# Kernel optimization log

Hardware: AMD Instinct MI355X
Metric: run time of the kernel (lower is better)

Reference implementation:

```python
import jax, jax.numpy as jnp
import numpy as np

D_MODEL = 1024
NUM_HEADS = 16
MAX_SEQ_LEN = 2048
BATCH = 4
SEQ_LEN = 2048


def setup_inputs() -> dict:
    key = jax.random.key(0)
    ks = jax.random.split(key, 7)
    s = 0.02
    return {
        "x": jax.random.normal(ks[0], (BATCH, SEQ_LEN, D_MODEL), dtype=jnp.float32),
        "Wq": jax.random.normal(ks[1], (D_MODEL, D_MODEL), dtype=jnp.float32) * s,
        "Wk": jax.random.normal(ks[2], (D_MODEL, D_MODEL), dtype=jnp.float32) * s,
        "Wv": jax.random.normal(ks[3], (D_MODEL, D_MODEL), dtype=jnp.float32) * s,
        "Wo": jax.random.normal(ks[4], (D_MODEL, D_MODEL), dtype=jnp.float32) * s,
        "bo": jnp.zeros((D_MODEL,), dtype=jnp.float32),
        "bias_table": jax.random.normal(ks[5], (2 * MAX_SEQ_LEN - 1, NUM_HEADS), dtype=jnp.float32) * s,
    }


def reference(x, Wq, Wk, Wv, Wo, bo, bias_table):
    B, S, D = x.shape
    H = NUM_HEADS
    hd = D // H
    scale = hd ** -0.5

    # torch Linear: y = x @ W.T
    q = (x @ Wq.T).reshape(B, S, H, hd).transpose(0, 2, 1, 3)  # [B,H,S,hd]
    k = (x @ Wk.T).reshape(B, S, H, hd).transpose(0, 2, 1, 3)
    v = (x @ Wv.T).reshape(B, S, H, hd).transpose(0, 2, 1, 3)

    scores = jnp.einsum("bhqd,bhkd->bhqk", q, k) * scale  # [B,H,S,S]

    # relative index: coords[:,None] - coords[None,:] + max_seq_len - 1
    coords = jnp.arange(S)
    rel_idx = coords[:, None] - coords[None, :] + MAX_SEQ_LEN - 1  # [S,S]
    rel_bias = bias_table[rel_idx]              # [S,S,H]
    rel_bias = rel_bias.transpose(2, 0, 1)[None]  # [1,H,S,S]

    probs = jax.nn.softmax(scores + rel_bias, axis=-1)
    ctx = jnp.einsum("bhqk,bhkd->bhqd", probs, v)  # [B,H,S,hd]
    ctx = ctx.transpose(0, 2, 1, 3).reshape(B, S, D)
    return ctx @ Wo.T + bo
```

## Files before the change

### kernel.cpp

```cpp
#include <hip/hip_runtime.h>
#include <string.h>

typedef unsigned short u16;
typedef unsigned int   u32;
typedef __attribute__((ext_vector_type(8))) short short8;
typedef __attribute__((ext_vector_type(4))) float f32x4;
typedef __attribute__((ext_vector_type(16))) float f32x16;
typedef __attribute__((ext_vector_type(2))) __fp16 h2;
typedef __attribute__((ext_vector_type(8))) __fp16 h8;
typedef __attribute__((ext_vector_type(2))) unsigned int u32x2;

__device__ __forceinline__ u16 f2b(float f) {
  u32 u = __float_as_uint(f);
  u32 r = (u + 0x7fffu + ((u >> 16) & 1u)) >> 16;
  return (u16)r;
}
__device__ __forceinline__ void cp16(const u16* g, u16* l) {
  __builtin_amdgcn_global_load_lds(
      (const __attribute__((address_space(1))) void*)g,
      (__attribute__((address_space(3))) void*)l, 16, 0, 0);
}
__device__ __forceinline__ void plswap(u32& a, u32& b) {
  u32x2 r = __builtin_amdgcn_permlane32_swap(a, b, false, false);
  a = r[0]; b = r[1];
}

__global__ __launch_bounds__(256) void cvt_f2b_kernel(const float* __restrict__ in,
                                                      u16* __restrict__ out, int n) {
  int i = (blockIdx.x * 256 + threadIdx.x) * 4;
  if (i + 3 < n) {
    float4 v = *(const float4*)&in[i];
    ushort4 o = make_ushort4(f2b(v.x), f2b(v.y), f2b(v.z), f2b(v.w));
    *(ushort4*)&out[i] = o;
  }
}
__global__ __launch_bounds__(256) void cvtw_kernel(const float* __restrict__ w0,
                                                   const float* __restrict__ w1,
                                                   const float* __restrict__ w2,
                                                   const float* __restrict__ w3,
                                                   u16* __restrict__ out) {
  const float* src = (blockIdx.y == 0) ? w0 : (blockIdx.y == 1) ? w1
                   : (blockIdx.y == 2) ? w2 : w3;
  int i = (blockIdx.x * 256 + threadIdx.x) * 4;
  float4 v = *(const float4*)&src[i];
  ushort4 o = make_ushort4(f2b(v.x), f2b(v.y), f2b(v.z), f2b(v.w));
  *(ushort4*)&out[(size_t)blockIdx.y * 1048576 + i] = o;
}

template<int MODE>
__global__ __launch_bounds__(256) void gemm128_bt(
    const u16* __restrict__ A, const u16* __restrict__ Bw,
    void* __restrict__ outp, const float* __restrict__ bias,
    const int M, const int N, const int K) {
  __shared__ __attribute__((aligned(16))) u16 As[2][128 * 32];
  __shared__ __attribute__((aligned(16))) u16 Bs[2][128 * 32];

  const u16* Bw2 = Bw;
  if (MODE == 0) Bw2 += ((size_t)blockIdx.z) << 20;

  const int tid  = threadIdx.x;
  const int wave = tid >> 6, lane = tid & 63;
  const int quad = lane >> 4, l15 = lane & 15;
  const int wm   = (wave >> 1) * 64, wn = (wave & 1) * 64;
  const int m0   = blockIdx.x * 128, n0 = blockIdx.y * 128;

  const int srow = wave * 32 + (lane >> 2);
  const int scol = (lane & 3) * 8;
  const u16* gA0 = A   + (size_t)(m0 + srow) * K + scol;
  const u16* gA1 = gA0 + (size_t)16 * K;
  const u16* gB0 = Bw2 + (size_t)(n0 + srow) * K + scol;
  const u16* gB1 = gB0 + (size_t)16 * K;
  const int lo0 = (wave * 32) * 32, lo1 = (wave * 32 + 16) * 32;

  cp16(gA0, &As[0][lo0]); cp16(gA1, &As[0][lo1]);
  cp16(gB0, &Bs[0][lo0]); cp16(gB1, &Bs[0][lo1]);
  gA0 += 32; gA1 += 32; gB0 += 32; gB1 += 32;

  f32x4 acc[4][4] = {};
  const int nk = K >> 5;
  for (int kt = 0; kt < nk; ++kt) {
    const int cur = kt & 1;
    __syncthreads();
    if (kt + 1 < nk) {
      cp16(gA0, &As[1 - cur][lo0]); cp16(gA1, &As[1 - cur][lo1]);
      cp16(gB0, &Bs[1 - cur][lo0]); cp16(gB1, &Bs[1 - cur][lo1]);
      gA0 += 32; gA1 += 32; gB0 += 32; gB1 += 32;
    }
    short8 af[4], bf[4];
    #pragma unroll
    for (int mi = 0; mi < 4; ++mi)
      af[mi] = *(const short8*)&As[cur][(wm + mi * 16 + l15) * 32 + quad * 8];
    #pragma unroll
    for (int ni = 0; ni < 4; ++ni)
      bf[ni] = *(const short8*)&Bs[cur][(wn + ni * 16 + l15) * 32 + quad * 8];
    #pragma unroll
    for (int mi = 0; mi < 4; ++mi)
      #pragma unroll
      for (int ni = 0; ni < 4; ++ni)
        acc[mi][ni] = __builtin_amdgcn_mfma_f32_16x16x32_bf16(af[mi], bf[ni], acc[mi][ni], 0, 0, 0);
  }

  #pragma unroll
  for (int mi = 0; mi < 4; ++mi)
    #pragma unroll
    for (int ni = 0; ni < 4; ++ni) {
      if (MODE == 0 && blockIdx.z == 2) {
        int mb = m0 + wm + mi * 16 + quad * 4;
        int n  = n0 + wn + ni * 16 + l15;
        int b = mb >> 11, s = mb & 2047, h = n >> 6, d = n & 63;
        u16* out = (u16*)outp + (((size_t)2) << 23);
        h2 p0 = __builtin_amdgcn_cvt_pkrtz(acc[mi][ni][0], acc[mi][ni][1]);
        h2 p1 = __builtin_amdgcn_cvt_pkrtz(acc[mi][ni][2], acc[mi][ni][3]);
        ushort4 o;
        memcpy(&o.x, &p0, 4);
        memcpy(&o.z, &p1, 4);
        *(ushort4*)&out[((((size_t)b * 16 + h) * 64 + d) << 11) + s] = o;
      } else {
        #pragma unroll
        for (int r = 0; r < 4; ++r) {
          int m = m0 + wm + mi * 16 + quad * 4 + r;
          int n = n0 + wn + ni * 16 + l15;
          float v = acc[mi][ni][r];
          if (MODE == 0) {
            int b = m >> 11, s = m & 2047, h = n >> 6, d = n & 63;
            u16* out = (u16*)outp + (((size_t)blockIdx.z) << 23);
            out[((((size_t)b * 16 + h) * 2048 + s) << 6) + d] = f2b(v);
          } else {
            ((float*)outp)[(size_t)m * N + n] = v + bias[n];
          }
        }
      }
    }
}

__global__ __launch_bounds__(256, 2) void attn_mfma_kernel(
    const u16* __restrict__ qb, const u16* __restrict__ kb, const u16* __restrict__ vtb,
    const float* __restrict__ bias_table, u16* __restrict__ ctx) {
  __shared__ __attribute__((aligned(16))) u16 Ks[2][64 * 64];
  __shared__ __attribute__((aligned(16))) u16 Vs[2][64 * 64];
  __shared__ __attribute__((aligned(16))) f32x4 bias4[2304];

  const int tid  = threadIdx.x;
  const int wave = tid >> 6, lane = tid & 63;
  const int l31  = lane & 31, hi = lane >> 5;
  const int xsw  = l31 & 7;
  const int bh   = blockIdx.x, h = bh & 15, b = bh >> 4;
  const int q0   = blockIdx.y * 256;

  {
    float* btmp = (float*)&Ks[0][0];
    for (int i = tid; i < 2304; i += 256) {
      int j = q0 + i; if (j > 4094) j = 4094;
      btmp[i] = bias_table[j * 16 + h] * 1.44269504f;
    }
    __syncthreads();
    for (int i = tid; i < 2304; i += 256) {
      f32x4 v;
      v[0] = btmp[i];
      v[1] = btmp[(i + 1) & 2047 ? (i + 1 < 2304 ? i + 1 : 2303) : (i + 1 < 2304 ? i + 1 : 2303)];
      v[1] = btmp[i + 1 < 2304 ? i + 1 : 2303];
      v[2] = btmp[i + 2 < 2304 ? i + 2 : 2303];
      v[3] = btmp[i + 3 < 2304 ? i + 3 : 2303];
      bias4[i] = v;
    }
    __syncthreads();
  }

  short8 aQ[2][4];
  #pragma unroll
  for (int qs = 0; qs < 2; ++qs)
    #pragma unroll
    for (int ks = 0; ks < 4; ++ks)
      aQ[qs][ks] = *(const short8*)&qb[((size_t)bh * 2048 + q0 + wave * 64 + qs * 32 + l31) * 64
                                       + ks * 16 + hi * 8];

  f32x16 accO[2][2] = {};
  f32x16 accL[2]    = {};

  const h8 ones8 = {(__fp16)1.f, (__fp16)1.f, (__fp16)1.f, (__fp16)1.f,
                    (__fp16)1.f, (__fp16)1.f, (__fp16)1.f, (__fp16)1.f};

  const int krow = lane >> 3;
  const int kchk = (lane & 7) ^ krow;
  const u16* kbase = kb + (((size_t)bh * 2048) << 6);

  const int srow = tid >> 2, t0 = tid & 3, ssw = srow & 7;
  const u16* vrow = vtb + (((size_t)bh * 64 + srow) << 11) + t0 * 16;
  const int vo0 = srow * 64 + (((2 * t0    ) ^ ssw) << 3);
  const int vo1 = srow * 64 + (((2 * t0 + 1) ^ ssw) << 3);

  short8 vpre0 = *(const short8*)&vrow[0];
  short8 vpre1 = *(const short8*)&vrow[8];
  *(short8*)&Vs[0][vo0] = vpre0;
  *(short8*)&Vs[0][vo1] = vpre1;
  #pragma unroll
  for (int g = 0; g < 2; ++g)
    cp16(kbase + (size_t)(wave * 16 + g * 8 + krow) * 64 + kchk * 8,
         &Ks[0][(wave * 16 + g * 8) * 64]);
  vpre0 = *(const short8*)&vrow[64];
  vpre1 = *(const short8*)&vrow[72];

  for (int kt = 0; kt < 32; ++kt) {
    const int cur = kt & 1;
    __syncthreads();
    if (kt < 31) {
      #pragma unroll
      for (int g = 0; g < 2; ++g)
        cp16(kbase + (size_t)((kt + 1) * 64 + wave * 16 + g * 8 + krow) * 64 + kchk * 8,
             &Ks[1 - cur][(wave * 16 + g * 8) * 64]);
      *(short8*)&Vs[1 - cur][vo0] = vpre0;
      *(short8*)&Vs[1 - cur][vo1] = vpre1;
      if (kt < 30) {
        const u16* vp = vrow + ((size_t)(kt + 2) << 6);
        vpre0 = *(const short8*)&vp[0];
        vpre1 = *(const short8*)&vp[8];
      }
    }

    #pragma unroll
    for (int t = 0; t < 2; ++t) {
      short8 aK[4];
      #pragma unroll
      for (int ks = 0; ks < 4; ++ks)
        aK[ks] = *(const short8*)&Ks[cur][(t * 32 + l31) * 64
                                          + (((ks * 2 + hi) ^ xsw) << 3)];
      f32x16 accS[2] = {};
      __builtin_amdgcn_s_setprio(1);
      #pragma unroll
      for (int ks = 0; ks < 4; ++ks)
        #pragma unroll
        for (int qs = 0; qs < 2; ++qs)
          accS[qs] = __builtin_amdgcn_mfma_f32_32x32x16_bf16(aK[ks], aQ[qs][ks], accS[qs], 0, 0, 0);
      __builtin_amdgcn_s_setprio(0);

      u32 d[2][8];
      #pragma unroll
      for (int qs = 0; qs < 2; ++qs) {
        const int ib3 = wave * 64 + qs * 32 + l31 - kt * 64 - t * 32 - 4 * hi + 2044;
        #pragma unroll
        for (int rg = 0; rg < 4; ++rg) {
          const f32x4 bb4 = bias4[ib3 - 8 * rg];
          float p0 = __builtin_amdgcn_exp2f(fmaf(accS[qs][4 * rg + 0], 0.18033688f, bb4[3]));
          float p1 = __builtin_amdgcn_exp2f(fmaf(accS[qs][4 * rg + 1], 0.18033688f, bb4[2]));
          float p2 = __builtin_amdgcn_exp2f(fmaf(accS[qs][4 * rg + 2], 0.18033688f, bb4[1]));
          float p3 = __builtin_amdgcn_exp2f(fmaf(accS[qs][4 * rg + 3], 0.18033688f, bb4[0]));
          h2 e0; e0[0] = (__fp16)p0; e0[1] = (__fp16)p1;
          h2 e1; e1[0] = (__fp16)p2; e1[1] = (__fp16)p3;
          memcpy(&d[qs][2 * rg],     &e0, 4);
          memcpy(&d[qs][2 * rg + 1], &e1, 4);
        }
      }

      #pragma unroll
      for (int sl = 0; sl < 2; ++sl) {
        const int ch = ((t * 2 + sl) * 2 + hi) ^ xsw;
        short8 av0 = *(const short8*)&Vs[cur][(     l31) * 64 + (ch << 3)];
        short8 av1 = *(const short8*)&Vs[cur][(32 + l31) * 64 + (ch << 3)];
        h8 avh0, avh1;
        memcpy(&avh0, &av0, 16);
        memcpy(&avh1, &av1, 16);
        __builtin_amdgcn_s_setprio(1);
        #pragma unroll
        for (int qs = 0; qs < 2; ++qs) {
          u32 F0 = d[qs][4 * sl], F1 = d[qs][4 * sl + 1];
          u32 F2 = d[qs][4 * sl + 2], F3 = d[qs][4 * sl + 3];
          plswap(F0, F2);
          plswap(F1, F3);
          union { u32 w[4]; h8 v; } uf;
          uf.w[0] = F0; uf.w[1] = F1; uf.w[2] = F2; uf.w[3] = F3;
          accO[qs][0] = __builtin_amdgcn_mfma_f32_32x32x16_f16(avh0, uf.v, accO[qs][0], 0, 0, 0);
          accO[qs][1] = __builtin_amdgcn_mfma_f32_32x32x16_f16(avh1, uf.v, accO[qs][1], 0, 0, 0);
          accL[qs]    = __builtin_amdgcn_mfma_f32_32x32x16_f16(ones8, uf.v, accL[qs], 0, 0, 0);
        }
        __builtin_amdgcn_s_setprio(0);
      }
    }
  }

  #pragma unroll
  for (int qs = 0; qs < 2; ++qs) {
    const float inv = 1.0f / accL[qs][0];
    const int q = q0 + wave * 64 + qs * 32 + l31;
    #pragma unroll
    for (int dt = 0; dt < 2; ++dt)
      #pragma unroll
      for (int rg = 0; rg < 4; ++rg) {
        ushort4 o = make_ushort4(f2b(accO[qs][dt][4 * rg + 0] * inv), f2b(accO[qs][dt][4 * rg + 1] * inv),
                                 f2b(accO[qs][dt][4 * rg + 2] * inv), f2b(accO[qs][dt][4 * rg + 3] * inv));
        *(ushort4*)&ctx[((size_t)b * 2048 + q) * 1024 + h * 64 + dt * 32 + rg * 8 + hi * 4] = o;
      }
  }
}

extern "C" void kernel_launch(void* const* d_in, const int* in_sizes, int n_in,
                              void* d_out, int out_size, void* d_ws, size_t ws_size,
                              hipStream_t stream) {
  const float* x          = (const float*)d_in[0];
  const float* Wq         = (const float*)d_in[1];
  const float* Wk         = (const float*)d_in[2];
  const float* Wv         = (const float*)d_in[3];
  const float* Wo         = (const float*)d_in[4];
  const float* bo         = (const float*)d_in[5];
  const float* bias_table = (const float*)d_in[6];
  float* out = (float*)d_out;

  char* ws = (char*)d_ws;
  u16* xb   = (u16*)(ws);
  u16* wqb  = (u16*)(ws + 16777216);
  u16* wob  = (u16*)(ws + 16777216 + 3 * 2097152);
  u16* qb   = (u16*)(ws + 25165824);
  u16* kb   = qb + 8388608;
  u16* vtb  = kb + 8388608;
  u16* ctxb = (u16*)(ws + 75497472);

  cvt_f2b_kernel<<<8192, 256, 0, stream>>>(x, xb, 8388608);
  cvtw_kernel<<<dim3(1024, 4), 256, 0, stream>>>(Wq, Wk, Wv, Wo, wqb);

  gemm128_bt<0><<<dim3(64, 8, 3), 256, 0, stream>>>(
      xb, wqb, (void*)qb, nullptr, 8192, 1024, 1024);

  attn_mfma_kernel<<<dim3(64, 8), 256, 0, stream>>>(qb, kb, vtb, bias_table, ctxb);

  gemm128_bt<1><<<dim3(64, 8), 256, 0, stream>>>(
      ctxb, wob, (void*)out, bo, 8192, 1024, 1024);
}
```

Baseline: 279.9 us.

## Stage QKV GEMM epilogue through swizzled LDS and remap block tiles

The QKV projection epilogue now writes each wave's 64x64 tile into a swizzled LDS buffer and then emits 16-byte vectorized global stores per lane, replacing the scattered 2-byte and 8-byte stores. Block indices are also remapped into 8x8 groups so that neighbouring blocks share A and B tiles in cache. The MODE 1 (output projection) path is split out unchanged. The staging costs an extra barrier and LDS round trip, and the tile remap hardcodes a 64-wide grid in x.

```diff
diff --git a/kernel.cpp b/kernel.cpp
--- a/kernel.cpp
+++ b/kernel.cpp
@@ -62,7 +62,11 @@
   const int wave = tid >> 6, lane = tid & 63;
   const int quad = lane >> 4, l15 = lane & 15;
   const int wm   = (wave >> 1) * 64, wn = (wave & 1) * 64;
-  const int m0   = blockIdx.x * 128, n0 = blockIdx.y * 128;
+
+  const int dlin = blockIdx.x + (blockIdx.y << 6);
+  const int xt   = ((dlin >> 6) << 3) + (dlin & 7);
+  const int yt   = (dlin >> 3) & 7;
+  const int m0   = xt * 128, n0 = yt * 128;
 
   const int srow = wave * 32 + (lane >> 2);
   const int scol = (lane & 3) * 8;
@@ -100,37 +104,68 @@
         acc[mi][ni] = __builtin_amdgcn_mfma_f32_16x16x32_bf16(af[mi], bf[ni], acc[mi][ni], 0, 0, 0);
   }
 
-  #pragma unroll
-  for (int mi = 0; mi < 4; ++mi)
-    #pragma unroll
-    for (int ni = 0; ni < 4; ++ni) {
-      if (MODE == 0 && blockIdx.z == 2) {
-        int mb = m0 + wm + mi * 16 + quad * 4;
-        int n  = n0 + wn + ni * 16 + l15;
-        int b = mb >> 11, s = mb & 2047, h = n >> 6, d = n & 63;
-        u16* out = (u16*)outp + (((size_t)2) << 23);
-        h2 p0 = __builtin_amdgcn_cvt_pkrtz(acc[mi][ni][0], acc[mi][ni][1]);
-        h2 p1 = __builtin_amdgcn_cvt_pkrtz(acc[mi][ni][2], acc[mi][ni][3]);
-        ushort4 o;
-        memcpy(&o.x, &p0, 4);
-        memcpy(&o.z, &p1, 4);
-        *(ushort4*)&out[((((size_t)b * 16 + h) * 64 + d) << 11) + s] = o;
-      } else {
+  if (MODE == 1) {
+    #pragma unroll
+    for (int mi = 0; mi < 4; ++mi)
+      #pragma unroll
+      for (int ni = 0; ni < 4; ++ni)
         #pragma unroll
         for (int r = 0; r < 4; ++r) {
           int m = m0 + wm + mi * 16 + quad * 4 + r;
           int n = n0 + wn + ni * 16 + l15;
-          float v = acc[mi][ni][r];
-          if (MODE == 0) {
-            int b = m >> 11, s = m & 2047, h = n >> 6, d = n & 63;
-            u16* out = (u16*)outp + (((size_t)blockIdx.z) << 23);
-            out[((((size_t)b * 16 + h) * 2048 + s) << 6) + d] = f2b(v);
-          } else {
-            ((float*)outp)[(size_t)m * N + n] = v + bias[n];
-          }
+          ((float*)outp)[(size_t)m * N + n] = acc[mi][ni][r] + bias[n];
         }
-      }
-    }
+    return;
+  }
+
+  __syncthreads();
+  u16* T = (wave == 0) ? &As[0][0] : (wave == 1) ? &As[1][0]
+         : (wave == 2) ? &Bs[0][0] : &Bs[1][0];
+
+  const int hh = (n0 + wn) >> 6;
+  const int mb = m0 + wm;
+  const int bb = mb >> 11;
+
+  if (blockIdx.z == 2) {
+    #pragma unroll
+    for (int mi = 0; mi < 4; ++mi)
+      #pragma unroll
+      for (int ni = 0; ni < 4; ++ni) {
+        h2 p0 = __builtin_amdgcn_cvt_pkrtz(acc[mi][ni][0], acc[mi][ni][1]);
+        h2 p1 = __builtin_amdgcn_cvt_pkrtz(acc[mi][ni][2], acc[mi][ni][3]);
+        int n = ni * 16 + l15, m = mi * 16 + quad * 4;
+        int byt = n * 128 + ((((m >> 3) ^ (n & 7)) << 4)) + ((m & 7) * 2);
+        uint2 w; memcpy(&w.x, &p0, 4); memcpy(&w.y, &p1, 4);
+        *(uint2*)((char*)T + byt) = w;
+      }
+    const int dl = lane;
+    u16* o = (u16*)outp + (((size_t)2) << 23)
+           + ((((size_t)bb * 16 + hh) * 64 + dl) << 11) + (mb & 2047);
+    #pragma unroll
+    for (int c = 0; c < 8; ++c) {
+      short8 v = *(short8*)((char*)T + dl * 128 + ((c ^ (dl & 7)) << 4));
+      *(short8*)&o[c * 8] = v;
+    }
+  } else {
+    #pragma unroll
+    for (int mi = 0; mi < 4; ++mi)
+      #pragma unroll
+      for (int ni = 0; ni < 4; ++ni)
+        #pragma unroll
+        for (int r = 0; r < 4; ++r) {
+          int m = mi * 16 + quad * 4 + r, n = ni * 16 + l15;
+          int byt = m * 128 + ((((n >> 3) ^ (m & 7)) << 4)) + ((n & 7) * 2);
+          *(u16*)((char*)T + byt) = f2b(acc[mi][ni][r]);
+        }
+    const int sl = lane;
+    u16* o = (u16*)outp + (((size_t)blockIdx.z) << 23)
+           + ((((size_t)bb * 16 + hh) * 2048 + ((mb + sl) & 2047)) << 6);
+    #pragma unroll
+    for (int c = 0; c < 8; ++c) {
+      short8 v = *(short8*)((char*)T + sl * 128 + ((c ^ (sl & 7)) << 4));
+      *(short8*)&o[c * 8] = v;
+    }
+  }
 }
 
 __global__ __launch_bounds__(256, 2) void attn_mfma_kernel(
@@ -157,7 +192,6 @@
     for (int i = tid; i < 2304; i += 256) {
       f32x4 v;
       v[0] = btmp[i];
-      v[1] = btmp[(i + 1) & 2047 ? (i + 1 < 2304 ? i + 1 : 2303) : (i + 1 < 2304 ? i + 1 : 2303)];
       v[1] = btmp[i + 1 < 2304 ? i + 1 : 2303];
       v[2] = btmp[i + 2 < 2304 ? i + 2 : 2303];
       v[3] = btmp[i + 3 < 2304 ? i + 3 : 2303];
```

Measured after the change: 290.8 us. 1.04x slower.
